# Kernel optimization log

Hardware: AMD Instinct MI355X
Metric: run time of the kernel (lower is better)

Reference implementation:

```python
import jax, jax.numpy as jnp
import numpy as np

K = 8  # number of nearest neighbors


def knn_graph(x, k):
    """Binary k-NN adjacency: A[i, j] = 1 iff j is among the k nearest
    neighbors of i (self excluded), matching torch cdist + topk + scatter."""
    n = x.shape[0]
    sq = jnp.sum(x * x, axis=1)  # [n]
    # Squared euclidean distances (same ordering as cdist for top-k).
    d = sq[:, None] + sq[None, :] - 2.0 * (x @ x.T)  # [n, n]
    # Exclude self by pushing the diagonal to +inf.
    d = d + jnp.where(jnp.eye(n, dtype=bool), jnp.inf, 0.0).astype(x.dtype)
    _, idx = jax.lax.top_k(-d, k)  # k smallest distances -> [n, k]
    rows = jnp.arange(n)[:, None]  # [n, 1]
    a = jnp.zeros((n, n), dtype=x.dtype).at[rows, idx].set(1.0)
    return a


def bce_mean(p, t):
    """F.binary_cross_entropy with reduction='mean'; torch clamps log at -100."""
    log_p = jnp.clip(jnp.log(p), -100.0)
    log_1mp = jnp.clip(jnp.log1p(-p), -100.0)
    return jnp.mean(-(t * log_p + (1.0 - t) * log_1mp))


def setup_inputs() -> dict:
    key = jax.random.key(0)
    kx, kz = jax.random.split(key)
    X = jax.random.normal(kx, (8192, 128), dtype=jnp.float32)
    Z = jax.random.normal(kz, (8192, 32), dtype=jnp.float32)
    return {"X": X, "Z": Z}


def reference(X, Z):
    A_X = knn_graph(X, K)
    A_Z = knn_graph(Z, K)
    return bce_mean(A_Z, A_X)
```

## Files before the change

### kernel.cpp

```cpp
#include <hip/hip_runtime.h>
#include <hip/hip_bf16.h>
#include <math.h>

#define N_PTS 8192
#define KNN 8
#define JSPLIT 16
#define WAVES 4
#define NQ 2
#define QT_PER_BLOCK (WAVES * NQ)
#define NTILE (N_PTS / 16)
#define NBX (NTILE / QT_PER_BLOCK)
#define JCHUNK (N_PTS / JSPLIT)
#define JTILES (JCHUNK / 16)
#define TB 2
#define NB (JTILES / TB)
#define NPART (NBX * JSPLIT)

typedef __attribute__((ext_vector_type(8))) short bf16x8;
typedef __attribute__((ext_vector_type(4))) float f32x4;

__device__ __forceinline__ float med3(float a, float b, float c) {
    return __builtin_amdgcn_fmed3f(a, b, c);
}

__device__ __forceinline__ void insertv(float v, float (&d)[8]) {
    float p = d[0];
    d[0] = fminf(v, d[0]);
#pragma unroll
    for (int k = 1; k < 8; ++k) {
        float q = d[k];
        d[k] = med3(v, p, q);
        p = q;
    }
}

template <int D>
__global__ __launch_bounds__(256) void prep_sq(const float* __restrict__ x,
                                               float* __restrict__ sq) {
    const int row = (blockIdx.x * 256 + threadIdx.x) >> 6;
    const int lane = threadIdx.x & 63;
    float s = 0.f;
    if constexpr (D == 128) {
        float2 v = *reinterpret_cast<const float2*>(x + (size_t)row * D + lane * 2);
        s = fmaf(v.x, v.x, v.y * v.y);
    } else {
        float v = (lane < D) ? x[(size_t)row * D + lane] : 0.f;
        s = v * v;
    }
#pragma unroll
    for (int o = 32; o > 0; o >>= 1) s += __shfl_down(s, o);
    if (lane == 0) sq[row] = s;
}

template <int D>
__global__ __launch_bounds__(256) void pack_kernel(const float* __restrict__ x,
                                                   bf16x8* __restrict__ pk) {
    constexpr int KB = D / 32;
    const int gid = blockIdx.x * 256 + threadIdx.x;
    const int l = gid & 63;
    const int kb = (gid >> 6) % KB;
    const int tile = gid / (64 * KB);
    const float* src = x + (size_t)(tile * 16 + (l & 15)) * D + kb * 32 + (l >> 4) * 8;
    bf16x8 v;
#pragma unroll
    for (int e = 0; e < 8; ++e) {
        __hip_bfloat16 h = __float2bfloat16(src[e]);
        v[e] = *reinterpret_cast<short*>(&h);
    }
    pk[gid] = v;
}

template <int D>
__global__ __launch_bounds__(256, 4) void thresh_scan(const bf16x8* __restrict__ pk,
                                                      const float* __restrict__ sq,
                                                      float* __restrict__ pd) {
    constexpr int KB = D / 32;
    constexpr int BCH = TB * KB * 64;
    __shared__ bf16x8 sbuf[2][BCH];
    __shared__ float lds_d[WAVES][NQ][64][8];

    const int t = threadIdx.x;
    const int lane = t & 63;
    const int w = __builtin_amdgcn_readfirstlane(t >> 6);
    const int qt0 = blockIdx.x * QT_PER_BLOCK + w * NQ;
    const int js = blockIdx.y;
    const int t0 = js * JTILES;
    const int lrow = lane & 15;
    const int jr = (lane >> 4) * 4;

    bf16x8 bfrag[NQ][KB];
#pragma unroll
    for (int q = 0; q < NQ; ++q)
#pragma unroll
        for (int kb = 0; kb < KB; ++kb)
            bfrag[q][kb] = pk[((size_t)(qt0 + q) * KB + kb) * 64 + lane];

    float d8[NQ][8];
#pragma unroll
    for (int q = 0; q < NQ; ++q)
#pragma unroll
        for (int k = 0; k < 8; ++k) d8[q][k] = __builtin_inff();

    {
        const size_t gb = (size_t)t0 * KB * 64;
        if constexpr (BCH == 512) {
            sbuf[0][t] = pk[gb + t];
            sbuf[0][t + 256] = pk[gb + t + 256];
        } else {
            if (t < BCH) sbuf[0][t] = pk[gb + t];
        }
    }
    __syncthreads();

    int cur = 0;
    bf16x8 stg0, stg1;
    for (int b = 0; b < NB; ++b) {
        if (b + 1 < NB) {
            const size_t gb = (size_t)(t0 + (b + 1) * TB) * KB * 64;
            if constexpr (BCH == 512) {
                stg0 = pk[gb + t];
                stg1 = pk[gb + t + 256];
            } else {
                if (t < BCH) stg0 = pk[gb + t];
            }
        }
#pragma unroll
        for (int u = 0; u < TB; ++u) {
            const int tt = t0 + b * TB + u;
            f32x4 acc[NQ];
#pragma unroll
            for (int q = 0; q < NQ; ++q) acc[q] = (f32x4){0.f, 0.f, 0.f, 0.f};
#pragma unroll
            for (int kb = 0; kb < KB; ++kb) {
                bf16x8 af = sbuf[cur][u * KB * 64 + kb * 64 + lane];
#pragma unroll
                for (int q = 0; q < NQ; ++q)
                    acc[q] = __builtin_amdgcn_mfma_f32_16x16x32_bf16(af, bfrag[q][kb], acc[q], 0, 0, 0);
            }
            f32x4 sq4 = *reinterpret_cast<const f32x4*>(sq + tt * 16 + jr);
#pragma unroll
            for (int q = 0; q < NQ; ++q) {
                if (tt == qt0 + q) {
#pragma unroll
                    for (int r = 0; r < 4; ++r) {
                        float dist = fmaf(-2.f, acc[q][r], sq4[r]);
                        if (jr + r == lrow) dist = __builtin_inff();
                        insertv(dist, d8[q]);
                    }
                } else {
#pragma unroll
                    for (int r = 0; r < 4; ++r) insertv(fmaf(-2.f, acc[q][r], sq4[r]), d8[q]);
                }
            }
        }
        if (b + 1 < NB) {
            if constexpr (BCH == 512) {
                sbuf[cur ^ 1][t] = stg0;
                sbuf[cur ^ 1][t + 256] = stg1;
            } else {
                if (t < BCH) sbuf[cur ^ 1][t] = stg0;
            }
        }
        __syncthreads();
        cur ^= 1;
    }

#pragma unroll
    for (int q = 0; q < NQ; ++q)
#pragma unroll
        for (int k = 0; k < 8; ++k) lds_d[w][q][lane][k] = d8[q][k];
    __syncthreads();
    if (t < QT_PER_BLOCK * 16) {
        const int bq = t >> 4;
        const int col = t & 15;
        const int w2 = bq >> 1;
        const int q2 = bq & 1;
        float e[8];
#pragma unroll
        for (int k = 0; k < 8; ++k) e[k] = lds_d[w2][q2][col][k];
#pragma unroll
        for (int p = 1; p < 4; ++p)
#pragma unroll
            for (int k = 0; k < 8; ++k) insertv(lds_d[w2][q2][p * 16 + col][k], e);
        const int row = (blockIdx.x * QT_PER_BLOCK + bq) * 16 + col;
        const size_t o = ((size_t)js * N_PTS + row) * 8;
#pragma unroll
        for (int k = 0; k < 8; ++k) pd[o + k] = e[k];
    }
}

__global__ __launch_bounds__(256) void thresh_merge(const float* __restrict__ pd,
                                                    float* __restrict__ t) {
    const int row = blockIdx.x * 256 + threadIdx.x;
    float d8[8];
#pragma unroll
    for (int k = 0; k < 8; ++k) d8[k] = __builtin_inff();
    for (int js = 0; js < JSPLIT; ++js) {
        const f32x4* p = reinterpret_cast<const f32x4*>(pd + ((size_t)js * N_PTS + row) * 8);
        f32x4 a = p[0], b = p[1];
        insertv(a[0], d8); insertv(a[1], d8); insertv(a[2], d8); insertv(a[3], d8);
        insertv(b[0], d8); insertv(b[1], d8); insertv(b[2], d8); insertv(b[3], d8);
    }
    t[row] = d8[7];
}

__global__ __launch_bounds__(256, 4) void count_scan(const bf16x8* __restrict__ pkX,
                                                     const float* __restrict__ sqX,
                                                     const float* __restrict__ tX,
                                                     const bf16x8* __restrict__ pkZ,
                                                     const float* __restrict__ sqZ,
                                                     const float* __restrict__ tZ,
                                                     int* __restrict__ partial) {
    __shared__ bf16x8 sbX[2][TB * 4 * 64];
    __shared__ bf16x8 sbZ[2][TB * 1 * 64];
    __shared__ int wsum[WAVES];

    const int t = threadIdx.x;
    const int lane = t & 63;
    const int w = __builtin_amdgcn_readfirstlane(t >> 6);
    const int qt0 = blockIdx.x * QT_PER_BLOCK + w * NQ;
    const int js = blockIdx.y;
    const int t0 = js * JTILES;
    const int lrow = lane & 15;
    const int jr = (lane >> 4) * 4;

    bf16x8 bfX[NQ][4];
    bf16x8 bfZ[NQ];
    float tx[NQ], tz[NQ];
#pragma unroll
    for (int q = 0; q < NQ; ++q) {
#pragma unroll
        for (int kb = 0; kb < 4; ++kb) bfX[q][kb] = pkX[((size_t)(qt0 + q) * 4 + kb) * 64 + lane];
        bfZ[q] = pkZ[(size_t)(qt0 + q) * 64 + lane];
        tx[q] = tX[(qt0 + q) * 16 + lrow];
        tz[q] = tZ[(qt0 + q) * 16 + lrow];
    }

    {
        const size_t gx = (size_t)t0 * 4 * 64;
        const size_t gz = (size_t)t0 * 64;
        sbX[0][t] = pkX[gx + t];
        sbX[0][t + 256] = pkX[gx + t + 256];
        if (t < TB * 64) sbZ[0][t] = pkZ[gz + t];
    }
    __syncthreads();

    int c = 0;
    int cur = 0;
    bf16x8 sx0, sx1, sz0;
    for (int b = 0; b < NB; ++b) {
        if (b + 1 < NB) {
            const size_t gx = (size_t)(t0 + (b + 1) * TB) * 4 * 64;
            const size_t gz = (size_t)(t0 + (b + 1) * TB) * 64;
            sx0 = pkX[gx + t];
            sx1 = pkX[gx + t + 256];
            if (t < TB * 64) sz0 = pkZ[gz + t];
        }
#pragma unroll
        for (int u = 0; u < TB; ++u) {
            const int tt = t0 + b * TB + u;
            f32x4 accX[NQ], accZ[NQ];
#pragma unroll
            for (int q = 0; q < NQ; ++q) {
                accX[q] = (f32x4){0.f, 0.f, 0.f, 0.f};
                accZ[q] = (f32x4){0.f, 0.f, 0.f, 0.f};
            }
#pragma unroll
            for (int kb = 0; kb < 4; ++kb) {
                bf16x8 af = sbX[cur][u * 4 * 64 + kb * 64 + lane];
#pragma unroll
                for (int q = 0; q < NQ; ++q)
                    accX[q] = __builtin_amdgcn_mfma_f32_16x16x32_bf16(af, bfX[q][kb], accX[q], 0, 0, 0);
            }
            {
                bf16x8 afZ = sbZ[cur][u * 64 + lane];
#pragma unroll
                for (int q = 0; q < NQ; ++q)
                    accZ[q] = __builtin_amdgcn_mfma_f32_16x16x32_bf16(afZ, bfZ[q], accZ[q], 0, 0, 0);
            }
            f32x4 sx4 = *reinterpret_cast<const f32x4*>(sqX + tt * 16 + jr);
            f32x4 sz4 = *reinterpret_cast<const f32x4*>(sqZ + tt * 16 + jr);
#pragma unroll
            for (int q = 0; q < NQ; ++q) {
                if (tt == qt0 + q) {
#pragma unroll
                    for (int r = 0; r < 4; ++r) {
                        float dx = fmaf(-2.f, accX[q][r], sx4[r]);
                        float dz = fmaf(-2.f, accZ[q][r], sz4[r]);
                        c += (dx <= tx[q] && dz <= tz[q] && (jr + r != lrow)) ? 1 : 0;
                    }
                } else {
#pragma unroll
                    for (int r = 0; r < 4; ++r) {
                        float dx = fmaf(-2.f, accX[q][r], sx4[r]);
                        float dz = fmaf(-2.f, accZ[q][r], sz4[r]);
                        c += (dx <= tx[q] && dz <= tz[q]) ? 1 : 0;
                    }
                }
            }
        }
        if (b + 1 < NB) {
            sbX[cur ^ 1][t] = sx0;
            sbX[cur ^ 1][t + 256] = sx1;
            if (t < TB * 64) sbZ[cur ^ 1][t] = sz0;
        }
        __syncthreads();
        cur ^= 1;
    }

#pragma unroll
    for (int o = 32; o > 0; o >>= 1) c += __shfl_down(c, o);
    if (lane == 0) wsum[w] = c;
    __syncthreads();
    if (t == 0)
        partial[blockIdx.y * NBX + blockIdx.x] = wsum[0] + wsum[1] + wsum[2] + wsum[3];
}

__global__ void finalize_kernel(const int* __restrict__ partial, float* __restrict__ out) {
    int v = 0;
    for (int k = threadIdx.x; k < NPART; k += 256) v += partial[k];
#pragma unroll
    for (int o = 32; o > 0; o >>= 1) v += __shfl_down(v, o);
    __shared__ int wsum[4];
    if ((threadIdx.x & 63) == 0) wsum[threadIdx.x >> 6] = v;
    __syncthreads();
    if (threadIdx.x == 0) {
        double m = (double)(wsum[0] + wsum[1] + wsum[2] + wsum[3]);
        out[0] = (float)((2.0 * KNN * N_PTS - 2.0 * m) * 100.0 / ((double)N_PTS * (double)N_PTS));
    }
}

extern "C" void kernel_launch(void* const* d_in, const int* in_sizes, int n_in,
                              void* d_out, int out_size, void* d_ws, size_t ws_size,
                              hipStream_t stream) {
    const float* X = (const float*)d_in[0];
    const float* Z = (const float*)d_in[1];
    float* out = (float*)d_out;
    char* ws = (char*)d_ws;

    bf16x8* pkX = (bf16x8*)(ws);
    bf16x8* pkZ = (bf16x8*)(ws + 2097152);
    float* sqX = (float*)(ws + 2621440);
    float* sqZ = (float*)(ws + 2654208);
    float* pdX = (float*)(ws + 2686976);
    float* pdZ = (float*)(ws + 11075584);
    float* tX = (float*)(ws + 19464192);
    float* tZ = (float*)(ws + 19496960);
    int* partial = (int*)(ws + 19529728);

    prep_sq<128><<<N_PTS / 4, 256, 0, stream>>>(X, sqX);
    prep_sq<32><<<N_PTS / 4, 256, 0, stream>>>(Z, sqZ);
    pack_kernel<128><<<NTILE * 4 * 64 / 256, 256, 0, stream>>>(X, pkX);
    pack_kernel<32><<<NTILE * 1 * 64 / 256, 256, 0, stream>>>(Z, pkZ);
    thresh_scan<128><<<dim3(NBX, JSPLIT), 256, 0, stream>>>(pkX, sqX, pdX);
    thresh_scan<32><<<dim3(NBX, JSPLIT), 256, 0, stream>>>(pkZ, sqZ, pdZ);
    thresh_merge<<<N_PTS / 256, 256, 0, stream>>>(pdX, tX);
    thresh_merge<<<N_PTS / 256, 256, 0, stream>>>(pdZ, tZ);
    count_scan<<<dim3(NBX, JSPLIT), 256, 0, stream>>>(pkX, sqX, tX, pkZ, sqZ, tZ, partial);
    finalize_kernel<<<1, 256, 0, stream>>>(partial, out);
}
```

Measured before the change: 167.4 us.

## Fuse X and Z threshold scans, coalesce packing via LDS, double staging tile

Merges the two per-dataset threshold-scan kernels into one kernel that computes X and Z distance tiles together, and fuses the two merge launches into one 2D grid. The pack kernel now reads float4-coalesced rows into LDS before emitting MFMA fragments. TB is raised from 2 to 4 so each LDS double buffer stages more j-tiles per barrier, with occupancy bound lowered to 3 waves-groups for the fused scan. The aim is fewer launches, fewer syncs, and better load coalescing, at the cost of more registers and LDS per block.

New measurement: 156.8 us. 6.4% less time.

```diff
diff --git a/kernel.cpp b/kernel.cpp
--- a/kernel.cpp
+++ b/kernel.cpp
@@ -10,9 +10,8 @@
 #define QT_PER_BLOCK (WAVES * NQ)
 #define NTILE (N_PTS / 16)
 #define NBX (NTILE / QT_PER_BLOCK)
-#define JCHUNK (N_PTS / JSPLIT)
-#define JTILES (JCHUNK / 16)
-#define TB 2
+#define JTILES ((N_PTS / JSPLIT) / 16)
+#define TB 4
 #define NB (JTILES / TB)
 #define NPART (NBX * JSPLIT)
 
@@ -56,28 +55,48 @@
 __global__ __launch_bounds__(256) void pack_kernel(const float* __restrict__ x,
                                                    bf16x8* __restrict__ pk) {
     constexpr int KB = D / 32;
-    const int gid = blockIdx.x * 256 + threadIdx.x;
-    const int l = gid & 63;
-    const int kb = (gid >> 6) % KB;
-    const int tile = gid / (64 * KB);
-    const float* src = x + (size_t)(tile * 16 + (l & 15)) * D + kb * 32 + (l >> 4) * 8;
-    bf16x8 v;
-#pragma unroll
-    for (int e = 0; e < 8; ++e) {
-        __hip_bfloat16 h = __float2bfloat16(src[e]);
-        v[e] = *reinterpret_cast<short*>(&h);
-    }
-    pk[gid] = v;
-}
-
-template <int D>
-__global__ __launch_bounds__(256, 4) void thresh_scan(const bf16x8* __restrict__ pk,
-                                                      const float* __restrict__ sq,
-                                                      float* __restrict__ pd) {
-    constexpr int KB = D / 32;
-    constexpr int BCH = TB * KB * 64;
-    __shared__ bf16x8 sbuf[2][BCH];
-    __shared__ float lds_d[WAVES][NQ][64][8];
+    constexpr int TPB = 2048 / (16 * D);
+    constexpr int PAD = 8;
+    __shared__ short lds[16 * TPB * (D + PAD)];
+    const int t = threadIdx.x;
+    const size_t base = (size_t)blockIdx.x * 2048;
+#pragma unroll
+    for (int h = 0; h < 2; ++h) {
+        const int fi = (t * 2 + h) * 4;
+        float4 v = *reinterpret_cast<const float4*>(x + base + fi);
+        const int row = fi / D;
+        const int col = fi % D;
+        short4 s;
+        __hip_bfloat16 b0 = __float2bfloat16(v.x);
+        __hip_bfloat16 b1 = __float2bfloat16(v.y);
+        __hip_bfloat16 b2 = __float2bfloat16(v.z);
+        __hip_bfloat16 b3 = __float2bfloat16(v.w);
+        s.x = *reinterpret_cast<short*>(&b0);
+        s.y = *reinterpret_cast<short*>(&b1);
+        s.z = *reinterpret_cast<short*>(&b2);
+        s.w = *reinterpret_cast<short*>(&b3);
+        *reinterpret_cast<short4*>(&lds[row * (D + PAD) + col]) = s;
+    }
+    __syncthreads();
+    const int tpb_idx = t / (KB * 64);
+    const int rem = t % (KB * 64);
+    const int kb = rem >> 6, l = rem & 63;
+    const int row = tpb_idx * 16 + (l & 15);
+    const int col = kb * 32 + (l >> 4) * 8;
+    bf16x8 v = *reinterpret_cast<const bf16x8*>(&lds[row * (D + PAD) + col]);
+    const int tile = blockIdx.x * TPB + tpb_idx;
+    pk[(size_t)(tile * KB + kb) * 64 + l] = v;
+}
+
+__global__ __launch_bounds__(256, 3) void thresh_scan_xz(const bf16x8* __restrict__ pkX,
+                                                         const float* __restrict__ sqX,
+                                                         float* __restrict__ pdX,
+                                                         const bf16x8* __restrict__ pkZ,
+                                                         const float* __restrict__ sqZ,
+                                                         float* __restrict__ pdZ) {
+    __shared__ char smem[40960];
+    bf16x8(*sbX)[TB * 4 * 64] = reinterpret_cast<bf16x8(*)[TB * 4 * 64]>(smem);
+    bf16x8(*sbZ)[TB * 64] = reinterpret_cast<bf16x8(*)[TB * 64]>(smem + 32768);
 
     const int t = threadIdx.x;
     const int lane = t & 63;
@@ -88,110 +107,129 @@
     const int lrow = lane & 15;
     const int jr = (lane >> 4) * 4;
 
-    bf16x8 bfrag[NQ][KB];
+    bf16x8 bfX[NQ][4];
+    bf16x8 bfZ[NQ];
+#pragma unroll
+    for (int q = 0; q < NQ; ++q) {
+#pragma unroll
+        for (int kb = 0; kb < 4; ++kb) bfX[q][kb] = pkX[((size_t)(qt0 + q) * 4 + kb) * 64 + lane];
+        bfZ[q] = pkZ[(size_t)(qt0 + q) * 64 + lane];
+    }
+
+    float d8x[NQ][8], d8z[NQ][8];
 #pragma unroll
     for (int q = 0; q < NQ; ++q)
 #pragma unroll
-        for (int kb = 0; kb < KB; ++kb)
-            bfrag[q][kb] = pk[((size_t)(qt0 + q) * KB + kb) * 64 + lane];
-
-    float d8[NQ][8];
-#pragma unroll
-    for (int q = 0; q < NQ; ++q)
-#pragma unroll
-        for (int k = 0; k < 8; ++k) d8[q][k] = __builtin_inff();
+        for (int k = 0; k < 8; ++k) { d8x[q][k] = __builtin_inff(); d8z[q][k] = __builtin_inff(); }
 
     {
-        const size_t gb = (size_t)t0 * KB * 64;
-        if constexpr (BCH == 512) {
-            sbuf[0][t] = pk[gb + t];
-            sbuf[0][t + 256] = pk[gb + t + 256];
-        } else {
-            if (t < BCH) sbuf[0][t] = pk[gb + t];
-        }
+        const size_t gx = (size_t)t0 * 4 * 64;
+        const size_t gz = (size_t)t0 * 64;
+#pragma unroll
+        for (int s = 0; s < 4; ++s) sbX[0][t + s * 256] = pkX[gx + t + s * 256];
+        sbZ[0][t] = pkZ[gz + t];
     }
     __syncthreads();
 
     int cur = 0;
-    bf16x8 stg0, stg1;
+    bf16x8 rx[4], rz;
     for (int b = 0; b < NB; ++b) {
         if (b + 1 < NB) {
-            const size_t gb = (size_t)(t0 + (b + 1) * TB) * KB * 64;
-            if constexpr (BCH == 512) {
-                stg0 = pk[gb + t];
-                stg1 = pk[gb + t + 256];
-            } else {
-                if (t < BCH) stg0 = pk[gb + t];
-            }
+            const size_t gx = (size_t)(t0 + (b + 1) * TB) * 4 * 64;
+            const size_t gz = (size_t)(t0 + (b + 1) * TB) * 64;
+#pragma unroll
+            for (int s = 0; s < 4; ++s) rx[s] = pkX[gx + t + s * 256];
+            rz = pkZ[gz + t];
         }
 #pragma unroll
         for (int u = 0; u < TB; ++u) {
             const int tt = t0 + b * TB + u;
-            f32x4 acc[NQ];
-#pragma unroll
-            for (int q = 0; q < NQ; ++q) acc[q] = (f32x4){0.f, 0.f, 0.f, 0.f};
-#pragma unroll
-            for (int kb = 0; kb < KB; ++kb) {
-                bf16x8 af = sbuf[cur][u * KB * 64 + kb * 64 + lane];
+            f32x4 accX[NQ], accZ[NQ];
+#pragma unroll
+            for (int q = 0; q < NQ; ++q) {
+                accX[q] = (f32x4){0.f, 0.f, 0.f, 0.f};
+                accZ[q] = (f32x4){0.f, 0.f, 0.f, 0.f};
+            }
+#pragma unroll
+            for (int kb = 0; kb < 4; ++kb) {
+                bf16x8 af = sbX[cur][u * 256 + kb * 64 + lane];
 #pragma unroll
                 for (int q = 0; q < NQ; ++q)
-                    acc[q] = __builtin_amdgcn_mfma_f32_16x16x32_bf16(af, bfrag[q][kb], acc[q], 0, 0, 0);
-            }
-            f32x4 sq4 = *reinterpret_cast<const f32x4*>(sq + tt * 16 + jr);
+                    accX[q] = __builtin_amdgcn_mfma_f32_16x16x32_bf16(af, bfX[q][kb], accX[q], 0, 0, 0);
+            }
+            {
+                bf16x8 afZ = sbZ[cur][u * 64 + lane];
+#pragma unroll
+                for (int q = 0; q < NQ; ++q)
+                    accZ[q] = __builtin_amdgcn_mfma_f32_16x16x32_bf16(afZ, bfZ[q], accZ[q], 0, 0, 0);
+            }
+            f32x4 sx4 = *reinterpret_cast<const f32x4*>(sqX + tt * 16 + jr);
+            f32x4 sz4 = *reinterpret_cast<const f32x4*>(sqZ + tt * 16 + jr);
 #pragma unroll
             for (int q = 0; q < NQ; ++q) {
                 if (tt == qt0 + q) {
 #pragma unroll
                     for (int r = 0; r < 4; ++r) {
-                        float dist = fmaf(-2.f, acc[q][r], sq4[r]);
-                        if (jr + r == lrow) dist = __builtin_inff();
-                        insertv(dist, d8[q]);
+                        float dx = fmaf(-2.f, accX[q][r], sx4[r]);
+                        float dz = fmaf(-2.f, accZ[q][r], sz4[r]);
+                        if (jr + r == lrow) { dx = __builtin_inff(); dz = __builtin_inff(); }
+                        insertv(dx, d8x[q]);
+                        insertv(dz, d8z[q]);
                     }
                 } else {
 #pragma unroll
-                    for (int r = 0; r < 4; ++r) insertv(fmaf(-2.f, acc[q][r], sq4[r]), d8[q]);
+                    for (int r = 0; r < 4; ++r) {
+                        insertv(fmaf(-2.f, accX[q][r], sx4[r]), d8x[q]);
+                        insertv(fmaf(-2.f, accZ[q][r], sz4[r]), d8z[q]);
+                    }
                 }
             }
         }
         if (b + 1 < NB) {
-            if constexpr (BCH == 512) {
-                sbuf[cur ^ 1][t] = stg0;
-                sbuf[cur ^ 1][t + 256] = stg1;
-            } else {
-                if (t < BCH) sbuf[cur ^ 1][t] = stg0;
-            }
+#pragma unroll
+            for (int s = 0; s < 4; ++s) sbX[cur ^ 1][t + s * 256] = rx[s];
+            sbZ[cur ^ 1][t] = rz;
         }
         __syncthreads();
         cur ^= 1;
     }
 
+    float(*ldsx)[NQ][64][8] = reinterpret_cast<float(*)[NQ][64][8]>(smem);
+    float(*ldsz)[NQ][64][8] = reinterpret_cast<float(*)[NQ][64][8]>(smem + 16384);
 #pragma unroll
     for (int q = 0; q < NQ; ++q)
 #pragma unroll
-        for (int k = 0; k < 8; ++k) lds_d[w][q][lane][k] = d8[q][k];
-    __syncthreads();
-    if (t < QT_PER_BLOCK * 16) {
-        const int bq = t >> 4;
-        const int col = t & 15;
-        const int w2 = bq >> 1;
-        const int q2 = bq & 1;
+        for (int k = 0; k < 8; ++k) { ldsx[w][q][lane][k] = d8x[q][k]; ldsz[w][q][lane][k] = d8z[q][k]; }
+    __syncthreads();
+    {
+        const int half = t >> 7;
+        const int u = t & 127;
+        const int bq = u >> 4;
+        const int col = u & 15;
+        const int w2 = bq >> 1, q2 = bq & 1;
+        const float(*src)[NQ][64][8] = half ? ldsz : ldsx;
         float e[8];
 #pragma unroll
-        for (int k = 0; k < 8; ++k) e[k] = lds_d[w2][q2][col][k];
+        for (int k = 0; k < 8; ++k) e[k] = src[w2][q2][col][k];
 #pragma unroll
         for (int p = 1; p < 4; ++p)
 #pragma unroll
-            for (int k = 0; k < 8; ++k) insertv(lds_d[w2][q2][p * 16 + col][k], e);
+            for (int k = 0; k < 8; ++k) insertv(src[w2][q2][p * 16 + col][k], e);
         const int row = (blockIdx.x * QT_PER_BLOCK + bq) * 16 + col;
+        float* pd = half ? pdZ : pdX;
         const size_t o = ((size_t)js * N_PTS + row) * 8;
 #pragma unroll
         for (int k = 0; k < 8; ++k) pd[o + k] = e[k];
     }
 }
 
-__global__ __launch_bounds__(256) void thresh_merge(const float* __restrict__ pd,
-                                                    float* __restrict__ t) {
+__global__ __launch_bounds__(256) void thresh_merge(const float* __restrict__ pdX,
+                                                    float* __restrict__ tXo,
+                                                    const float* __restrict__ pdZ,
+                                                    float* __restrict__ tZo) {
     const int row = blockIdx.x * 256 + threadIdx.x;
+    const float* pd = blockIdx.y ? pdZ : pdX;
+    float* to = blockIdx.y ? tZo : tXo;
     float d8[8];
 #pragma unroll
     for (int k = 0; k < 8; ++k) d8[k] = __builtin_inff();
@@ -201,7 +239,7 @@
         insertv(a[0], d8); insertv(a[1], d8); insertv(a[2], d8); insertv(a[3], d8);
         insertv(b[0], d8); insertv(b[1], d8); insertv(b[2], d8); insertv(b[3], d8);
     }
-    t[row] = d8[7];
+    to[row] = d8[7];
 }
 
 __global__ __launch_bounds__(256, 4) void count_scan(const bf16x8* __restrict__ pkX,
@@ -211,8 +249,9 @@
                                                      const float* __restrict__ sqZ,
                                                      const float* __restrict__ tZ,
                                                      int* __restrict__ partial) {
-    __shared__ bf16x8 sbX[2][TB * 4 * 64];
-    __shared__ bf16x8 sbZ[2][TB * 1 * 64];
+    __shared__ char smem[40960];
+    bf16x8(*sbX)[TB * 4 * 64] = reinterpret_cast<bf16x8(*)[TB * 4 * 64]>(smem);
+    bf16x8(*sbZ)[TB * 64] = reinterpret_cast<bf16x8(*)[TB * 64]>(smem + 32768);
     __shared__ int wsum[WAVES];
 
     const int t = threadIdx.x;
@@ -239,22 +278,22 @@
     {
         const size_t gx = (size_t)t0 * 4 * 64;
         const size_t gz = (size_t)t0 * 64;
-        sbX[0][t] = pkX[gx + t];
-        sbX[0][t + 256] = pkX[gx + t + 256];
-        if (t < TB * 64) sbZ[0][t] = pkZ[gz + t];
+#pragma unroll
+        for (int s = 0; s < 4; ++s) sbX[0][t + s * 256] = pkX[gx + t + s * 256];
+        sbZ[0][t] = pkZ[gz + t];
     }
     __syncthreads();
 
     int c = 0;
     int cur = 0;
-    bf16x8 sx0, sx1, sz0;
+    bf16x8 rx[4], rz;
     for (int b = 0; b < NB; ++b) {
         if (b + 1 < NB) {
             const size_t gx = (size_t)(t0 + (b + 1) * TB) * 4 * 64;
             const size_t gz = (size_t)(t0 + (b + 1) * TB) * 64;
-            sx0 = pkX[gx + t];
-            sx1 = pkX[gx + t + 256];
-            if (t < TB * 64) sz0 = pkZ[gz + t];
+#pragma unroll
+            for (int s = 0; s < 4; ++s) rx[s] = pkX[gx + t + s * 256];
+            rz = pkZ[gz + t];
         }
 #pragma unroll
         for (int u = 0; u < TB; ++u) {
@@ -267,7 +306,7 @@
             }
 #pragma unroll
             for (int kb = 0; kb < 4; ++kb) {
-                bf16x8 af = sbX[cur][u * 4 * 64 + kb * 64 + lane];
+                bf16x8 af = sbX[cur][u * 256 + kb * 64 + lane];
 #pragma unroll
                 for (int q = 0; q < NQ; ++q)
                     accX[q] = __builtin_amdgcn_mfma_f32_16x16x32_bf16(af, bfX[q][kb], accX[q], 0, 0, 0);
@@ -300,9 +339,9 @@
             }
         }
         if (b + 1 < NB) {
-            sbX[cur ^ 1][t] = sx0;
-            sbX[cur ^ 1][t + 256] = sx1;
-            if (t < TB * 64) sbZ[cur ^ 1][t] = sz0;
+#pragma unroll
+            for (int s = 0; s < 4; ++s) sbX[cur ^ 1][t + s * 256] = rx[s];
+            sbZ[cur ^ 1][t] = rz;
         }
         __syncthreads();
         cur ^= 1;
@@ -350,12 +389,10 @@
 
     prep_sq<128><<<N_PTS / 4, 256, 0, stream>>>(X, sqX);
     prep_sq<32><<<N_PTS / 4, 256, 0, stream>>>(Z, sqZ);
-    pack_kernel<128><<<NTILE * 4 * 64 / 256, 256, 0, stream>>>(X, pkX);
-    pack_kernel<32><<<NTILE * 1 * 64 / 256, 256, 0, stream>>>(Z, pkZ);
-    thresh_scan<128><<<dim3(NBX, JSPLIT), 256, 0, stream>>>(pkX, sqX, pdX);
-    thresh_scan<32><<<dim3(NBX, JSPLIT), 256, 0, stream>>>(pkZ, sqZ, pdZ);
-    thresh_merge<<<N_PTS / 256, 256, 0, stream>>>(pdX, tX);
-    thresh_merge<<<N_PTS / 256, 256, 0, stream>>>(pdZ, tZ);
+    pack_kernel<128><<<NTILE, 256, 0, stream>>>(X, pkX);
+    pack_kernel<32><<<NTILE / 4, 256, 0, stream>>>(Z, pkZ);
+    thresh_scan_xz<<<dim3(NBX, JSPLIT), 256, 0, stream>>>(pkX, sqX, pdX, pkZ, sqZ, pdZ);
+    thresh_merge<<<dim3(N_PTS / 256, 2), 256, 0, stream>>>(pdX, tX, pdZ, tZ);
     count_scan<<<dim3(NBX, JSPLIT), 256, 0, stream>>>(pkX, sqX, tX, pkZ, sqZ, tZ, partial);
     finalize_kernel<<<1, 256, 0, stream>>>(partial, out);
 }
```
